# Kernel optimization log

Measured on AMD Instinct MI355X. Metric: run time of the kernel, lower is better.

The kernel has to match this reference:

```python
import jax, jax.numpy as jnp
import numpy as np

B, L, IN_DIM, H, KD = 2, 2048, 1024, 16, 64
SCALE = float(np.sqrt(IN_DIM / H))  # sqrt(in_dim / num_heads), per ScaledDotAttention
LN_EPS = 1e-5


def setup_inputs() -> dict:
    key = jax.random.key(0)
    ks = jax.random.split(key, 12)
    s_in = 1.0 / np.sqrt(IN_DIM)
    s_hd = 1.0 / np.sqrt(H * KD)
    return {
        "q": jax.random.normal(ks[0], (B, L, IN_DIM), jnp.float32),
        "k": jax.random.normal(ks[1], (B, L, IN_DIM), jnp.float32),
        "v": jax.random.normal(ks[2], (B, L, IN_DIM), jnp.float32),
        "Wq": jax.random.normal(ks[3], (IN_DIM, H * KD), jnp.float32) * s_in,
        "bq": jnp.zeros((H * KD,), jnp.float32),
        "Wk": jax.random.normal(ks[4], (IN_DIM, H * KD), jnp.float32) * s_in,
        "bk": jnp.zeros((H * KD,), jnp.float32),
        "Wv": jax.random.normal(ks[5], (IN_DIM, H * KD), jnp.float32) * s_in,
        "bv": jnp.zeros((H * KD,), jnp.float32),
        "Wo": jax.random.normal(ks[6], (H * KD, IN_DIM), jnp.float32) * s_hd,
        "bo": jnp.zeros((IN_DIM,), jnp.float32),
        "gamma": jnp.ones((IN_DIM,), jnp.float32),
        "beta": jnp.zeros((IN_DIM,), jnp.float32),
    }


def _split_heads(x):
    # [B, L, H*KD] -> [H*B, L, KD]  (heads MAJOR, matching permute(2,0,1,3).view)
    b, l, _ = x.shape
    return x.reshape(b, l, H, KD).transpose(2, 0, 1, 3).reshape(H * b, l, KD)


def reference(q, k, v, Wq, bq, Wk, bk, Wv, bv, Wo, bo, gamma, beta):
    res = q
    qh = _split_heads(q @ Wq + bq)   # [H*B, Lq, KD]
    kh = _split_heads(k @ Wk + bk)
    vh = _split_heads(v @ Wv + bv)
    scores = jnp.einsum("zqd,zkd->zqk", qh, kh) / SCALE
    atn = jax.nn.softmax(scores, axis=-1)          # [H*B, Lq, Lk]
    out = jnp.einsum("zqk,zkd->zqd", atn, vh)      # [H*B, Lq, KD]
    b = q.shape[0]
    out = out.reshape(H, b, -1, KD).transpose(1, 2, 0, 3).reshape(b, -1, H * KD)
    out = out @ Wo + bo
    x = out + res
    mu = jnp.mean(x, axis=-1, keepdims=True)
    var = jnp.mean(jnp.square(x - mu), axis=-1, keepdims=True)
    out = (x - mu) * jax.lax.rsqrt(var + LN_EPS) * gamma + beta
    return (out, atn)
```

## Files before the change

### kernel.cpp

```cpp
#include <hip/hip_runtime.h>
#include <hip/hip_bf16.h>

typedef unsigned short u16;
typedef unsigned int   u32;

using bf16x8 = __attribute__((ext_vector_type(8))) short;
using f32x4  = __attribute__((ext_vector_type(4))) float;

#define SEQ  2048
#define NZ   32
#define KTOT 1024
#define NTOT 1024
#define SC2  0.18033688011112042f

__device__ __forceinline__ u16 f2bf(float f) {
    union { float f; u32 u; } x; x.f = f;
    u32 r = x.u + 0x7fffu + ((x.u >> 16) & 1u);
    return (u16)(r >> 16);
}

__device__ __forceinline__ void gl_lds16(const u16* g, u16* ldsbase) {
    __builtin_amdgcn_global_load_lds(
        (const __attribute__((address_space(1))) u32*)g,
        (__attribute__((address_space(3))) u32*)ldsbase, 16, 0, 0);
}

__global__ __launch_bounds__(256) void prep_k(const float* __restrict__ q,
                                              const float* __restrict__ k,
                                              const float* __restrict__ v,
                                              const float* __restrict__ W0,
                                              const float* __restrict__ W1,
                                              const float* __restrict__ W2,
                                              const float* __restrict__ W3,
                                              u16* __restrict__ qb,
                                              u16* __restrict__ WT) {
    __shared__ u16 t[64 * 65];
    const int tid = threadIdx.x;
    const int b = blockIdx.x;
    if (b < 6144) {
        const int zc = b >> 11;
        const int xc = b & 2047;
        const float* src = (zc == 0) ? q : (zc == 1) ? k : v;
        u16* dst = qb + (size_t)zc * 4096 * 1024;
        int off = xc * 2048 + tid * 8;
        float4 v0 = *(const float4*)&src[off];
        float4 v1 = *(const float4*)&src[off + 4];
        uint4 o;
        o.x = (u32)f2bf(v0.x) | ((u32)f2bf(v0.y) << 16);
        o.y = (u32)f2bf(v0.z) | ((u32)f2bf(v0.w) << 16);
        o.z = (u32)f2bf(v1.x) | ((u32)f2bf(v1.y) << 16);
        o.w = (u32)f2bf(v1.z) | ((u32)f2bf(v1.w) << 16);
        *(uint4*)&dst[off] = o;
        return;
    }
    const int tt = b - 6144;
    const int zz = tt >> 8;
    const int bx = tt & 15, by = (tt >> 4) & 15;
    const float* W = (zz == 0) ? W0 : (zz == 1) ? W1 : (zz == 2) ? W2 : W3;
    u16* out = WT + (size_t)zz * 1024 * 1024;
    const int n0 = bx * 64, k0 = by * 64;
#pragma unroll
    for (int it = 0; it < 4; ++it) {
        int flat = it * 256 + tid;
        int r = flat >> 4, c4 = (flat & 15) * 4;
        float4 vv = *(const float4*)&W[(k0 + r) * 1024 + n0 + c4];
        t[r * 65 + c4 + 0] = f2bf(vv.x);
        t[r * 65 + c4 + 1] = f2bf(vv.y);
        t[r * 65 + c4 + 2] = f2bf(vv.z);
        t[r * 65 + c4 + 3] = f2bf(vv.w);
    }
    __syncthreads();
#pragma unroll
    for (int it = 0; it < 2; ++it) {
        int flat = it * 256 + tid;
        int rn = flat >> 3, c8 = (flat & 7) * 8;
        u32 p[4];
#pragma unroll
        for (int e = 0; e < 4; ++e) {
            u32 lo = t[(c8 + 2 * e + 0) * 65 + rn];
            u32 hi = t[(c8 + 2 * e + 1) * 65 + rn];
            p[e] = lo | (hi << 16);
        }
        uint4 o; o.x = p[0]; o.y = p[1]; o.z = p[2]; o.w = p[3];
        *(uint4*)&out[(n0 + rn) * 1024 + k0 + c8] = o;
    }
}

__global__ __launch_bounds__(256) void qkvproj_k(const u16* __restrict__ qb,
                                                 const u16* __restrict__ wt,
                                                 const float* __restrict__ bq,
                                                 const float* __restrict__ bk,
                                                 const float* __restrict__ bv,
                                                 u16* __restrict__ qh,
                                                 u16* __restrict__ kh,
                                                 u16* __restrict__ vhT) {
    __shared__ u16 As[128 * 32];
    __shared__ u16 Bs[128 * 32];
    __shared__ u16 T[128 * 132];
    const int zz = blockIdx.z;
    const u16*   A    = qb + (size_t)zz * 4096 * 1024;
    const u16*   WT   = wt + (size_t)zz * 1024 * 1024;
    const float* bias = (zz == 0) ? bq : (zz == 1) ? bk : bv;
    const bool vmode = (zz == 2);

    const int tid = threadIdx.x;
    const int m0 = blockIdx.y * 128;
    const int n0 = blockIdx.x * 128;
    const int wid = tid >> 6, lane = tid & 63;
    const int wrow = wid >> 1, wcol = wid & 1;
    const int g = lane >> 4, li = lane & 15;

    f32x4 acc[4][4];
#pragma unroll
    for (int a = 0; a < 4; ++a)
#pragma unroll
        for (int b = 0; b < 4; ++b) acc[a][b] = (f32x4){0.f, 0.f, 0.f, 0.f};

    for (int kt = 0; kt < KTOT / 32; ++kt) {
        const int kb = kt * 32;
#pragma unroll
        for (int cc = 0; cc < 2; ++cc) {
            int c = wid + cc * 4;
            gl_lds16(&A[(m0 + c * 16 + (lane >> 2)) * KTOT + kb + (lane & 3) * 8],
                     &As[c * 512]);
            gl_lds16(&WT[(n0 + c * 16 + (lane >> 2)) * KTOT + kb + (lane & 3) * 8],
                     &Bs[c * 512]);
        }
        __syncthreads();
        bf16x8 af[4], bfr[4];
#pragma unroll
        for (int fr = 0; fr < 4; ++fr)
            af[fr] = *(const bf16x8*)&As[(wrow * 64 + fr * 16 + li) * 32 + g * 8];
#pragma unroll
        for (int fc = 0; fc < 4; ++fc)
            bfr[fc] = *(const bf16x8*)&Bs[(wcol * 64 + fc * 16 + li) * 32 + g * 8];
#pragma unroll
        for (int fr = 0; fr < 4; ++fr)
#pragma unroll
            for (int fc = 0; fc < 4; ++fc)
                acc[fr][fc] = __builtin_amdgcn_mfma_f32_16x16x32_bf16(
                    af[fr], bfr[fc], acc[fr][fc], 0, 0, 0);
        __syncthreads();
    }

#pragma unroll
    for (int fr = 0; fr < 4; ++fr)
#pragma unroll
        for (int fc = 0; fc < 4; ++fc)
#pragma unroll
            for (int reg = 0; reg < 4; ++reg) {
                int rl = wrow * 64 + fr * 16 + g * 4 + reg;
                int cl = wcol * 64 + fc * 16 + li;
                u16 bv16 = f2bf(acc[fr][fc][reg] + bias[n0 + cl]);
                if (!vmode) T[rl * 132 + cl] = bv16;
                else        T[cl * 132 + rl] = bv16;
            }
    __syncthreads();

    const int bb2 = m0 >> 11, ml = m0 & 2047;
    const int lc8 = (tid & 7) * 8;
#pragma unroll
    for (int it = 0; it < 8; ++it) {
        int idx = it * 32 + (tid >> 3);
        int row = idx >> 1, half = idx & 1;
        uint4 val = *(const uint4*)&T[row * 132 + half * 64 + lc8];
        if (!vmode) {
            int h = (n0 >> 6) + half;
            u16* dst = (blockIdx.z == 0) ? qh : kh;
            *(uint4*)&dst[(((h * 2 + bb2) * 2048 + ml + row) << 6) + lc8] = val;
        } else {
            int cg = n0 + row;
            int h = cg >> 6, d = cg & 63;
            *(uint4*)&vhT[(((h * 2 + bb2) * 64 + d) << 11) + ml + half * 64 + lc8] = val;
        }
    }
}

__global__ __launch_bounds__(256) void outproj_k(const u16* __restrict__ A,
                                                 const u16* __restrict__ WT,
                                                 const float* __restrict__ bias,
                                                 const float* __restrict__ res,
                                                 float* __restrict__ outp) {
    __shared__ u16 As[128 * 32];
    __shared__ u16 Bs[128 * 32];
    const int tid = threadIdx.x;
    const int m0 = blockIdx.y * 128;
    const int n0 = blockIdx.x * 128;
    const int wid = tid >> 6, lane = tid & 63;
    const int wrow = wid >> 1, wcol = wid & 1;
    const int g = lane >> 4, li = lane & 15;

    f32x4 acc[4][4];
#pragma unroll
    for (int a = 0; a < 4; ++a)
#pragma unroll
        for (int b = 0; b < 4; ++b) acc[a][b] = (f32x4){0.f, 0.f, 0.f, 0.f};

    for (int kt = 0; kt < KTOT / 32; ++kt) {
        const int kb = kt * 32;
#pragma unroll
        for (int cc = 0; cc < 2; ++cc) {
            int c = wid + cc * 4;
            gl_lds16(&A[(m0 + c * 16 + (lane >> 2)) * KTOT + kb + (lane & 3) * 8],
                     &As[c * 512]);
            gl_lds16(&WT[(n0 + c * 16 + (lane >> 2)) * KTOT + kb + (lane & 3) * 8],
                     &Bs[c * 512]);
        }
        __syncthreads();
        bf16x8 af[4], bfr[4];
#pragma unroll
        for (int fr = 0; fr < 4; ++fr)
            af[fr] = *(const bf16x8*)&As[(wrow * 64 + fr * 16 + li) * 32 + g * 8];
#pragma unroll
        for (int fc = 0; fc < 4; ++fc)
            bfr[fc] = *(const bf16x8*)&Bs[(wcol * 64 + fc * 16 + li) * 32 + g * 8];
#pragma unroll
        for (int fr = 0; fr < 4; ++fr)
#pragma unroll
            for (int fc = 0; fc < 4; ++fc)
                acc[fr][fc] = __builtin_amdgcn_mfma_f32_16x16x32_bf16(
                    af[fr], bfr[fc], acc[fr][fc], 0, 0, 0);
        __syncthreads();
    }

#pragma unroll
    for (int fr = 0; fr < 4; ++fr)
#pragma unroll
        for (int fc = 0; fc < 4; ++fc)
#pragma unroll
            for (int reg = 0; reg < 4; ++reg) {
                int r = m0 + wrow * 64 + fr * 16 + g * 4 + reg;
                int c = n0 + wcol * 64 + fc * 16 + li;
                outp[r * NTOT + c] = acc[fr][fc][reg] + bias[c] + res[r * NTOT + c];
            }
}

__global__ __launch_bounds__(512) void attn_k(const u16* __restrict__ qh,
                                              const u16* __restrict__ kh,
                                              const u16* __restrict__ vhT,
                                              float* __restrict__ atn,
                                              u16* __restrict__ attnout) {
    __shared__ u16 lds[24576];
    const int tid = threadIdx.x;
    const int D = blockIdx.x;
    const int z = D & 31, q0 = (D >> 5) * 128;
    const int h = z >> 1, bb = z & 1;
    const int wid = tid >> 6, lane = tid & 63, g = lane >> 4, li = lane & 15;
    const int row0 = wid * 16;
    const int zbase = z * SEQ;
    const int swz = li & 7;

    bf16x8 aq[2];
#pragma unroll
    for (int ks = 0; ks < 2; ++ks)
        aq[ks] = *(const bf16x8*)
            &qh[(size_t)(zbase + q0 + row0 + li) * 64 + ks * 32 + g * 8];

    float lmv;
    {
        u16* KsA = lds;
        const int c0 = wid * 2, c1 = wid * 2 + 1;
        const int ar = lane >> 3;
        const int ac = (lane & 7) ^ ar;
        const u16* kA0 = &kh[(size_t)(zbase + c0 * 8 + ar) * 64 + ac * 8];
        const u16* kA1 = &kh[(size_t)(zbase + c1 * 8 + ar) * 64 + ac * 8];

        gl_lds16(kA0, &KsA[c0 * 512]);
        gl_lds16(kA1, &KsA[c1 * 512]);
        __syncthreads();

        float s = 0.f;
        for (int kt = 0; kt < 16; ++kt) {
            const int buf = kt & 1;
            if (kt < 15) {
                const size_t nxt = (size_t)(kt + 1) * 128 * 64;
                gl_lds16(kA0 + nxt, &KsA[(buf ^ 1) * 8192 + c0 * 512]);
                gl_lds16(kA1 + nxt, &KsA[(buf ^ 1) * 8192 + c1 * 512]);
            }
            f32x4 sv[8];
#pragma unroll
            for (int fc = 0; fc < 8; ++fc) sv[fc] = (f32x4){0.f, 0.f, 0.f, 0.f};
            __builtin_amdgcn_s_setprio(1);
#pragma unroll
            for (int ks = 0; ks < 2; ++ks) {
#pragma unroll
                for (int fc = 0; fc < 8; ++fc) {
                    bf16x8 kf = *(const bf16x8*)
                        &KsA[buf * 8192 + (fc * 16 + li) * 64 + (((ks * 4 + g) ^ swz) * 8)];
                    sv[fc] = __builtin_amdgcn_mfma_f32_16x16x32_bf16(
                        kf, aq[ks], sv[fc], 0, 0, 0);
                }
            }
            __builtin_amdgcn_s_setprio(0);
            float ssum = 0.f;
#pragma unroll
            for (int fc = 0; fc < 8; ++fc)
#pragma unroll
                for (int reg = 0; reg < 4; ++reg)
                    ssum += __builtin_amdgcn_exp2f(sv[fc][reg] * SC2);
            s += ssum;
            __syncthreads();
        }
        s += __shfl_xor(s, 16, 64);
        s += __shfl_xor(s, 32, 64);
        lmv = __builtin_amdgcn_logf(s);
    }

    u16* Ks = lds;
    u16* Vs = lds + 8192;
    u16* Ps = lds + 16384;
    const int srow = wid * 8 + (lane >> 3);
    const int schunk = (lane & 7) ^ (lane >> 3);
    const u16* ksrc = &kh[(size_t)(zbase + srow) * 64 + schunk * 8];
    const u16* vsrc = &vhT[(size_t)(z * 64 + srow) * SEQ + schunk * 8];

    gl_lds16(ksrc, &Ks[wid * 512]);
    gl_lds16(vsrc, &Vs[wid * 512]);
    __syncthreads();

    f32x4 oa[4];
#pragma unroll
    for (int fn = 0; fn < 4; ++fn) oa[fn] = (f32x4){0.f, 0.f, 0.f, 0.f};

    const u16* psw = &Ps[wid * 1024];
    const int prow = wid * 1024 + li * 64;
    for (int kt = 0; kt < 32; ++kt) {
        const int buf = kt & 1;
        const int k0 = kt * 64;
        if (kt < 31) {
            const size_t nxt = (size_t)((kt + 1) * 64);
            gl_lds16(ksrc + nxt * 64, &Ks[(buf ^ 1) * 4096 + wid * 512]);
            gl_lds16(vsrc + nxt, &Vs[(buf ^ 1) * 4096 + wid * 512]);
        }

        f32x4 sv[4];
#pragma unroll
        for (int fc = 0; fc < 4; ++fc) sv[fc] = (f32x4){0.f, 0.f, 0.f, 0.f};
        __builtin_amdgcn_s_setprio(1);
#pragma unroll
        for (int ks = 0; ks < 2; ++ks) {
#pragma unroll
            for (int fc = 0; fc < 4; ++fc) {
                bf16x8 kf = *(const bf16x8*)
                    &Ks[buf * 4096 + (fc * 16 + li) * 64 + (((ks * 4 + g) ^ swz) * 8)];
                sv[fc] = __builtin_amdgcn_mfma_f32_16x16x32_bf16(
                    kf, aq[ks], sv[fc], 0, 0, 0);
            }
        }
        __builtin_amdgcn_s_setprio(0);

#pragma unroll
        for (int fc = 0; fc < 4; ++fc) {
            float p0 = __builtin_amdgcn_exp2f(sv[fc][0] * SC2 - lmv);
            float p1 = __builtin_amdgcn_exp2f(sv[fc][1] * SC2 - lmv);
            float p2 = __builtin_amdgcn_exp2f(sv[fc][2] * SC2 - lmv);
            float p3 = __builtin_amdgcn_exp2f(sv[fc][3] * SC2 - lmv);
            u32 w0 = (u32)f2bf(p0) | ((u32)f2bf(p1) << 16);
            u32 w1 = (u32)f2bf(p2) | ((u32)f2bf(p3) << 16);
            int pc = ((fc * 2 + (g >> 1)) ^ swz) * 8 + (g & 1) * 4;
            *(u32*)&Ps[prow + pc]     = w0;
            *(u32*)&Ps[prow + pc + 2] = w1;
        }

#pragma unroll
        for (int it2 = 0; it2 < 4; ++it2) {
            int row  = it2 * 4 + (lane >> 4);
            int col8 = lane & 15;
            int lc   = col8 >> 1;
            uint2 d2 = *(const uint2*)
                &psw[row * 64 + ((lc ^ (row & 7)) << 3) + ((col8 & 1) << 2)];
            f32x4 o4;
            union { u32 u; float f; } c0v, c1v, c2v, c3v;
            c0v.u = (d2.x & 0xffffu) << 16;  c1v.u = d2.x & 0xffff0000u;
            c2v.u = (d2.y & 0xffffu) << 16;  c3v.u = d2.y & 0xffff0000u;
            o4[0] = c0v.f; o4[1] = c1v.f; o4[2] = c2v.f; o4[3] = c3v.f;
            __builtin_nontemporal_store(o4, (f32x4*)
                &atn[(size_t)(zbase + q0 + row0 + row) * SEQ + k0 + col8 * 4]);
        }

        __builtin_amdgcn_s_setprio(1);
#pragma unroll
        for (int ks = 0; ks < 2; ++ks) {
            bf16x8 pf = *(const bf16x8*)&Ps[prow + (((ks * 4 + g) ^ swz) * 8)];
#pragma unroll
            for (int fn = 0; fn < 4; ++fn) {
                bf16x8 vf = *(const bf16x8*)
                    &Vs[buf * 4096 + (fn * 16 + li) * 64 + (((ks * 4 + g) ^ swz) * 8)];
                oa[fn] = __builtin_amdgcn_mfma_f32_16x16x32_bf16(
                    vf, pf, oa[fn], 0, 0, 0);
            }
        }
        __builtin_amdgcn_s_setprio(0);
        asm volatile("s_waitcnt vmcnt(4) lgkmcnt(0)" ::: "memory");
        __builtin_amdgcn_s_barrier();
    }

#pragma unroll
    for (int fn = 0; fn < 4; ++fn) {
        u32 w0 = (u32)f2bf(oa[fn][0]) | ((u32)f2bf(oa[fn][1]) << 16);
        u32 w1 = (u32)f2bf(oa[fn][2]) | ((u32)f2bf(oa[fn][3]) << 16);
        uint2 wv; wv.x = w0; wv.y = w1;
        *(uint2*)&attnout[(size_t)(bb * SEQ + q0 + row0 + li) * 1024
                          + h * 64 + fn * 16 + g * 4] = wv;
    }
}

__global__ __launch_bounds__(256) void ln_k(const float* __restrict__ y,
                                            const float* __restrict__ gamma,
                                            const float* __restrict__ beta,
                                            float* __restrict__ out) {
    __shared__ float red[8];
    const int row = blockIdx.x, tid = threadIdx.x;
    float4 v = *(const float4*)&y[row * 1024 + tid * 4];
    float s = v.x + v.y + v.z + v.w;
    float sq = v.x * v.x + v.y * v.y + v.z * v.z + v.w * v.w;
#pragma unroll
    for (int msk = 1; msk <= 32; msk <<= 1) {
        s += __shfl_xor(s, msk, 64);
        sq += __shfl_xor(sq, msk, 64);
    }
    const int wid = tid >> 6;
    if ((tid & 63) == 0) { red[wid * 2] = s; red[wid * 2 + 1] = sq; }
    __syncthreads();
    s = red[0] + red[2] + red[4] + red[6];
    sq = red[1] + red[3] + red[5] + red[7];
    float mu = s * (1.0f / 1024.0f);
    float var = sq * (1.0f / 1024.0f) - mu * mu;
    float rs = rsqrtf(var + 1e-5f);
    float4 g4 = *(const float4*)&gamma[tid * 4];
    float4 b4 = *(const float4*)&beta[tid * 4];
    float4 o;
    o.x = (v.x - mu) * rs * g4.x + b4.x;
    o.y = (v.y - mu) * rs * g4.y + b4.y;
    o.z = (v.z - mu) * rs * g4.z + b4.z;
    o.w = (v.w - mu) * rs * g4.w + b4.w;
    *(float4*)&out[row * 1024 + tid * 4] = o;
}

extern "C" void kernel_launch(void* const* d_in, const int* in_sizes, int n_in,
                              void* d_out, int out_size, void* d_ws, size_t ws_size,
                              hipStream_t stream) {
    const float* q     = (const float*)d_in[0];
    const float* k     = (const float*)d_in[1];
    const float* v     = (const float*)d_in[2];
    const float* Wq    = (const float*)d_in[3];
    const float* bq    = (const float*)d_in[4];
    const float* Wk    = (const float*)d_in[5];
    const float* bk    = (const float*)d_in[6];
    const float* Wv    = (const float*)d_in[7];
    const float* bv    = (const float*)d_in[8];
    const float* Wo    = (const float*)d_in[9];
    const float* bo    = (const float*)d_in[10];
    const float* gamma = (const float*)d_in[11];
    const float* beta  = (const float*)d_in[12];

    float* out = (float*)d_out;
    float* atn = out + 4096 * 1024;

    u16* wt  = (u16*)d_ws;
    u16* qb  = wt + 4 * 1024 * 1024;
    u16* attnout = qb;
    float* y = (float*)(qb + 4096 * 1024);
    u16* qh  = qb + 3 * 4096 * 1024;
    u16* kh  = qh + NZ * SEQ * 64;
    u16* vhT = kh + NZ * SEQ * 64;
    u16* wto = wt + 3 * 1024 * 1024;

    dim3 tb(256);
    prep_k<<<dim3(7168), tb, 0, stream>>>(q, k, v, Wq, Wk, Wv, Wo, qb, wt);

    qkvproj_k<<<dim3(8, 32, 3), tb, 0, stream>>>(qb, wt, bq, bk, bv,
                                                 qh, kh, vhT);

    attn_k<<<dim3(512), dim3(512), 0, stream>>>(qh, kh, vhT, atn, attnout);

    outproj_k<<<dim3(8, 32), tb, 0, stream>>>(attnout, wto, bo, q, y);

    ln_k<<<dim3(4096), tb, 0, stream>>>(y, gamma, beta, out);
}
```

Measured before the change: 262.1 us.

## Load K/V fragments directly into registers and process two query sets per warp

The attention kernel stops staging K and V tiles in LDS through global_load_lds with barriers. Each warp now loads K/V MFMA fragments straight from global memory into registers, prefetching the next tile. Each warp handles 32 query rows (two 16-row sets) so every loaded K/V fragment feeds two MFMA streams, and the grid halves to 256 blocks with occupancy 2. This removes block-wide barriers and LDS traffic, but it increases global/L2 loads per warp and register pressure, and exposes fewer blocks on a large GPU.

```diff
diff --git a/kernel.cpp b/kernel.cpp
--- a/kernel.cpp
+++ b/kernel.cpp
@@ -23,6 +23,47 @@
     __builtin_amdgcn_global_load_lds(
         (const __attribute__((address_space(1))) u32*)g,
         (__attribute__((address_space(3))) u32*)ldsbase, 16, 0, 0);
+}
+
+__device__ __forceinline__ void ldk8(bf16x8 (&dst)[2][4], const u16* kbase,
+                                     int krow0, int klo) {
+#pragma unroll
+    for (int ks = 0; ks < 2; ++ks)
+#pragma unroll
+        for (int fc = 0; fc < 4; ++fc)
+            dst[ks][fc] = *(const bf16x8*)
+                &kbase[(size_t)(krow0 + fc * 16) * 64 + ks * 32 + klo];
+}
+
+__device__ __forceinline__ void passa_half(const bf16x8 (&kr)[2][4],
+                                           const bf16x8 (&aq)[2][2],
+                                           float& s0, float& s1) {
+    f32x4 sv0[4], sv1[4];
+#pragma unroll
+    for (int fc = 0; fc < 4; ++fc) {
+        sv0[fc] = (f32x4){0.f, 0.f, 0.f, 0.f};
+        sv1[fc] = (f32x4){0.f, 0.f, 0.f, 0.f};
+    }
+    __builtin_amdgcn_s_setprio(1);
+#pragma unroll
+    for (int ks = 0; ks < 2; ++ks)
+#pragma unroll
+        for (int fc = 0; fc < 4; ++fc) {
+            sv0[fc] = __builtin_amdgcn_mfma_f32_16x16x32_bf16(
+                kr[ks][fc], aq[0][ks], sv0[fc], 0, 0, 0);
+            sv1[fc] = __builtin_amdgcn_mfma_f32_16x16x32_bf16(
+                kr[ks][fc], aq[1][ks], sv1[fc], 0, 0, 0);
+        }
+    __builtin_amdgcn_s_setprio(0);
+    float a0 = 0.f, a1 = 0.f;
+#pragma unroll
+    for (int fc = 0; fc < 4; ++fc)
+#pragma unroll
+        for (int reg = 0; reg < 4; ++reg) {
+            a0 += __builtin_amdgcn_exp2f(sv0[fc][reg] * SC2);
+            a1 += __builtin_amdgcn_exp2f(sv1[fc][reg] * SC2);
+        }
+    s0 += a0; s1 += a1;
 }
 
 __global__ __launch_bounds__(256) void prep_k(const float* __restrict__ q,
@@ -235,174 +276,178 @@
             }
 }
 
-__global__ __launch_bounds__(512) void attn_k(const u16* __restrict__ qh,
-                                              const u16* __restrict__ kh,
-                                              const u16* __restrict__ vhT,
-                                              float* __restrict__ atn,
-                                              u16* __restrict__ attnout) {
-    __shared__ u16 lds[24576];
+__global__ __launch_bounds__(512, 2) void attn_k(const u16* __restrict__ qh,
+                                                 const u16* __restrict__ kh,
+                                                 const u16* __restrict__ vhT,
+                                                 float* __restrict__ atn,
+                                                 u16* __restrict__ attnout) {
+    __shared__ u16 Ps[8 * 2048];
     const int tid = threadIdx.x;
     const int D = blockIdx.x;
-    const int z = D & 31, q0 = (D >> 5) * 128;
+    const int z = D & 31, q0 = (D >> 5) * 256;
     const int h = z >> 1, bb = z & 1;
     const int wid = tid >> 6, lane = tid & 63, g = lane >> 4, li = lane & 15;
-    const int row0 = wid * 16;
+    const int row0 = wid * 32;
     const int zbase = z * SEQ;
     const int swz = li & 7;
 
-    bf16x8 aq[2];
-#pragma unroll
-    for (int ks = 0; ks < 2; ++ks)
-        aq[ks] = *(const bf16x8*)
-            &qh[(size_t)(zbase + q0 + row0 + li) * 64 + ks * 32 + g * 8];
-
-    float lmv;
+    const u16* kbase = kh + (size_t)zbase * 64;
+    const u16* vbase = vhT + (size_t)(z * 64) * SEQ;
+    const int klo = li * 64 + g * 8;
+    const int vlo = li * SEQ + g * 8;
+
+    bf16x8 aq[2][2];
+#pragma unroll
+    for (int set = 0; set < 2; ++set)
+#pragma unroll
+        for (int ks = 0; ks < 2; ++ks)
+            aq[set][ks] = *(const bf16x8*)
+                &qh[(size_t)(zbase + q0 + row0 + set * 16 + li) * 64
+                    + ks * 32 + g * 8];
+
+    float lmv0, lmv1;
     {
-        u16* KsA = lds;
-        const int c0 = wid * 2, c1 = wid * 2 + 1;
-        const int ar = lane >> 3;
-        const int ac = (lane & 7) ^ ar;
-        const u16* kA0 = &kh[(size_t)(zbase + c0 * 8 + ar) * 64 + ac * 8];
-        const u16* kA1 = &kh[(size_t)(zbase + c1 * 8 + ar) * 64 + ac * 8];
-
-        gl_lds16(kA0, &KsA[c0 * 512]);
-        gl_lds16(kA1, &KsA[c1 * 512]);
-        __syncthreads();
-
-        float s = 0.f;
-        for (int kt = 0; kt < 16; ++kt) {
-            const int buf = kt & 1;
-            if (kt < 15) {
-                const size_t nxt = (size_t)(kt + 1) * 128 * 64;
-                gl_lds16(kA0 + nxt, &KsA[(buf ^ 1) * 8192 + c0 * 512]);
-                gl_lds16(kA1 + nxt, &KsA[(buf ^ 1) * 8192 + c1 * 512]);
-            }
-            f32x4 sv[8];
-#pragma unroll
-            for (int fc = 0; fc < 8; ++fc) sv[fc] = (f32x4){0.f, 0.f, 0.f, 0.f};
-            __builtin_amdgcn_s_setprio(1);
-#pragma unroll
-            for (int ks = 0; ks < 2; ++ks) {
-#pragma unroll
-                for (int fc = 0; fc < 8; ++fc) {
-                    bf16x8 kf = *(const bf16x8*)
-                        &KsA[buf * 8192 + (fc * 16 + li) * 64 + (((ks * 4 + g) ^ swz) * 8)];
-                    sv[fc] = __builtin_amdgcn_mfma_f32_16x16x32_bf16(
-                        kf, aq[ks], sv[fc], 0, 0, 0);
-                }
-            }
-            __builtin_amdgcn_s_setprio(0);
-            float ssum = 0.f;
-#pragma unroll
-            for (int fc = 0; fc < 8; ++fc)
-#pragma unroll
-                for (int reg = 0; reg < 4; ++reg)
-                    ssum += __builtin_amdgcn_exp2f(sv[fc][reg] * SC2);
-            s += ssum;
-            __syncthreads();
-        }
-        s += __shfl_xor(s, 16, 64);
-        s += __shfl_xor(s, 32, 64);
-        lmv = __builtin_amdgcn_logf(s);
-    }
-
-    u16* Ks = lds;
-    u16* Vs = lds + 8192;
-    u16* Ps = lds + 16384;
-    const int srow = wid * 8 + (lane >> 3);
-    const int schunk = (lane & 7) ^ (lane >> 3);
-    const u16* ksrc = &kh[(size_t)(zbase + srow) * 64 + schunk * 8];
-    const u16* vsrc = &vhT[(size_t)(z * 64 + srow) * SEQ + schunk * 8];
-
-    gl_lds16(ksrc, &Ks[wid * 512]);
-    gl_lds16(vsrc, &Vs[wid * 512]);
-    __syncthreads();
-
-    f32x4 oa[4];
-#pragma unroll
-    for (int fn = 0; fn < 4; ++fn) oa[fn] = (f32x4){0.f, 0.f, 0.f, 0.f};
-
-    const u16* psw = &Ps[wid * 1024];
-    const int prow = wid * 1024 + li * 64;
+        float s0 = 0.f, s1 = 0.f;
+        bf16x8 ka[2][4], kb[2][4];
+        ldk8(ka, kbase, 0, klo);
+        for (int kt = 0; kt < 32; kt += 2) {
+            ldk8(kb, kbase, (kt + 1) * 64, klo);
+            passa_half(ka, aq, s0, s1);
+            if (kt < 30) ldk8(ka, kbase, (kt + 2) * 64, klo);
+            passa_half(kb, aq, s0, s1);
+        }
+        s0 += __shfl_xor(s0, 16, 64);
+        s0 += __shfl_xor(s0, 32, 64);
+        s1 += __shfl_xor(s1, 16, 64);
+        s1 += __shfl_xor(s1, 32, 64);
+        lmv0 = __builtin_amdgcn_logf(s0);
+        lmv1 = __builtin_amdgcn_logf(s1);
+    }
+
+    f32x4 oa[2][4];
+#pragma unroll
+    for (int set = 0; set < 2; ++set)
+#pragma unroll
+        for (int fn = 0; fn < 4; ++fn) oa[set][fn] = (f32x4){0.f, 0.f, 0.f, 0.f};
+
+    const int prow0 = wid * 2048 + li * 64;
+    const int prow1 = prow0 + 1024;
+    const int pswb  = wid * 2048;
+
+    bf16x8 kf[2][4], vf[2][4];
+    ldk8(kf, kbase, 0, klo);
+
     for (int kt = 0; kt < 32; ++kt) {
-        const int buf = kt & 1;
         const int k0 = kt * 64;
-        if (kt < 31) {
-            const size_t nxt = (size_t)((kt + 1) * 64);
-            gl_lds16(ksrc + nxt * 64, &Ks[(buf ^ 1) * 4096 + wid * 512]);
-            gl_lds16(vsrc + nxt, &Vs[(buf ^ 1) * 4096 + wid * 512]);
-        }
 
         f32x4 sv[4];
 #pragma unroll
         for (int fc = 0; fc < 4; ++fc) sv[fc] = (f32x4){0.f, 0.f, 0.f, 0.f};
         __builtin_amdgcn_s_setprio(1);
 #pragma unroll
-        for (int ks = 0; ks < 2; ++ks) {
-#pragma unroll
-            for (int fc = 0; fc < 4; ++fc) {
-                bf16x8 kf = *(const bf16x8*)
-                    &Ks[buf * 4096 + (fc * 16 + li) * 64 + (((ks * 4 + g) ^ swz) * 8)];
+        for (int ks = 0; ks < 2; ++ks)
+#pragma unroll
+            for (int fc = 0; fc < 4; ++fc)
                 sv[fc] = __builtin_amdgcn_mfma_f32_16x16x32_bf16(
-                    kf, aq[ks], sv[fc], 0, 0, 0);
-            }
-        }
+                    kf[ks][fc], aq[0][ks], sv[fc], 0, 0, 0);
         __builtin_amdgcn_s_setprio(0);
-
 #pragma unroll
         for (int fc = 0; fc < 4; ++fc) {
-            float p0 = __builtin_amdgcn_exp2f(sv[fc][0] * SC2 - lmv);
-            float p1 = __builtin_amdgcn_exp2f(sv[fc][1] * SC2 - lmv);
-            float p2 = __builtin_amdgcn_exp2f(sv[fc][2] * SC2 - lmv);
-            float p3 = __builtin_amdgcn_exp2f(sv[fc][3] * SC2 - lmv);
+            float p0 = __builtin_amdgcn_exp2f(sv[fc][0] * SC2 - lmv0);
+            float p1 = __builtin_amdgcn_exp2f(sv[fc][1] * SC2 - lmv0);
+            float p2 = __builtin_amdgcn_exp2f(sv[fc][2] * SC2 - lmv0);
+            float p3 = __builtin_amdgcn_exp2f(sv[fc][3] * SC2 - lmv0);
             u32 w0 = (u32)f2bf(p0) | ((u32)f2bf(p1) << 16);
             u32 w1 = (u32)f2bf(p2) | ((u32)f2bf(p3) << 16);
             int pc = ((fc * 2 + (g >> 1)) ^ swz) * 8 + (g & 1) * 4;
-            *(u32*)&Ps[prow + pc]     = w0;
-            *(u32*)&Ps[prow + pc + 2] = w1;
-        }
-
-#pragma unroll
-        for (int it2 = 0; it2 < 4; ++it2) {
-            int row  = it2 * 4 + (lane >> 4);
-            int col8 = lane & 15;
-            int lc   = col8 >> 1;
-            uint2 d2 = *(const uint2*)
-                &psw[row * 64 + ((lc ^ (row & 7)) << 3) + ((col8 & 1) << 2)];
-            f32x4 o4;
-            union { u32 u; float f; } c0v, c1v, c2v, c3v;
-            c0v.u = (d2.x & 0xffffu) << 16;  c1v.u = d2.x & 0xffff0000u;
-            c2v.u = (d2.y & 0xffffu) << 16;  c3v.u = d2.y & 0xffff0000u;
-            o4[0] = c0v.f; o4[1] = c1v.f; o4[2] = c2v.f; o4[3] = c3v.f;
-            __builtin_nontemporal_store(o4, (f32x4*)
-                &atn[(size_t)(zbase + q0 + row0 + row) * SEQ + k0 + col8 * 4]);
-        }
-
+            *(u32*)&Ps[prow0 + pc]     = w0;
+            *(u32*)&Ps[prow0 + pc + 2] = w1;
+        }
+
+        f32x4 sw[4];
+#pragma unroll
+        for (int fc = 0; fc < 4; ++fc) sw[fc] = (f32x4){0.f, 0.f, 0.f, 0.f};
         __builtin_amdgcn_s_setprio(1);
 #pragma unroll
+        for (int ks = 0; ks < 2; ++ks)
+#pragma unroll
+            for (int fc = 0; fc < 4; ++fc)
+                sw[fc] = __builtin_amdgcn_mfma_f32_16x16x32_bf16(
+                    kf[ks][fc], aq[1][ks], sw[fc], 0, 0, 0);
+        __builtin_amdgcn_s_setprio(0);
+
+#pragma unroll
+        for (int ks = 0; ks < 2; ++ks)
+#pragma unroll
+            for (int fn = 0; fn < 4; ++fn)
+                vf[ks][fn] = *(const bf16x8*)
+                    &vbase[(size_t)(fn * 16) * SEQ + vlo + k0 + ks * 32];
+        if (kt < 31) ldk8(kf, kbase, k0 + 64, klo);
+
+#pragma unroll
+        for (int fc = 0; fc < 4; ++fc) {
+            float p0 = __builtin_amdgcn_exp2f(sw[fc][0] * SC2 - lmv1);
+            float p1 = __builtin_amdgcn_exp2f(sw[fc][1] * SC2 - lmv1);
+            float p2 = __builtin_amdgcn_exp2f(sw[fc][2] * SC2 - lmv1);
+            float p3 = __builtin_amdgcn_exp2f(sw[fc][3] * SC2 - lmv1);
+            u32 w0 = (u32)f2bf(p0) | ((u32)f2bf(p1) << 16);
+            u32 w1 = (u32)f2bf(p2) | ((u32)f2bf(p3) << 16);
+            int pc = ((fc * 2 + (g >> 1)) ^ swz) * 8 + (g & 1) * 4;
+            *(u32*)&Ps[prow1 + pc]     = w0;
+            *(u32*)&Ps[prow1 + pc + 2] = w1;
+        }
+
+#pragma unroll
+        for (int set = 0; set < 2; ++set) {
+#pragma unroll
+            for (int it2 = 0; it2 < 4; ++it2) {
+                int row  = it2 * 4 + (lane >> 4);
+                int col8 = lane & 15;
+                int lc   = col8 >> 1;
+                uint2 d2 = *(const uint2*)
+                    &Ps[pswb + set * 1024 + row * 64
+                        + ((lc ^ (row & 7)) << 3) + ((col8 & 1) << 2)];
+                f32x4 o4;
+                union { u32 u; float f; } c0v, c1v, c2v, c3v;
+                c0v.u = (d2.x & 0xffffu) << 16;  c1v.u = d2.x & 0xffff0000u;
+                c2v.u = (d2.y & 0xffffu) << 16;  c3v.u = d2.y & 0xffff0000u;
+                o4[0] = c0v.f; o4[1] = c1v.f; o4[2] = c2v.f; o4[3] = c3v.f;
+                __builtin_nontemporal_store(o4, (f32x4*)
+                    &atn[(size_t)(zbase + q0 + row0 + set * 16 + row) * SEQ
+                         + k0 + col8 * 4]);
+            }
+        }
+
+        __builtin_amdgcn_s_setprio(1);
+#pragma unroll
         for (int ks = 0; ks < 2; ++ks) {
-            bf16x8 pf = *(const bf16x8*)&Ps[prow + (((ks * 4 + g) ^ swz) * 8)];
-#pragma unroll
-            for (int fn = 0; fn < 4; ++fn) {
-                bf16x8 vf = *(const bf16x8*)
-                    &Vs[buf * 4096 + (fn * 16 + li) * 64 + (((ks * 4 + g) ^ swz) * 8)];
-                oa[fn] = __builtin_amdgcn_mfma_f32_16x16x32_bf16(
-                    vf, pf, oa[fn], 0, 0, 0);
-            }
+            bf16x8 pf0 = *(const bf16x8*)&Ps[prow0 + (((ks * 4 + g) ^ swz) * 8)];
+#pragma unroll
+            for (int fn = 0; fn < 4; ++fn)
+                oa[0][fn] = __builtin_amdgcn_mfma_f32_16x16x32_bf16(
+                    vf[ks][fn], pf0, oa[0][fn], 0, 0, 0);
+        }
+#pragma unroll
+        for (int ks = 0; ks < 2; ++ks) {
+            bf16x8 pf1 = *(const bf16x8*)&Ps[prow1 + (((ks * 4 + g) ^ swz) * 8)];
+#pragma unroll
+            for (int fn = 0; fn < 4; ++fn)
+                oa[1][fn] = __builtin_amdgcn_mfma_f32_16x16x32_bf16(
+                    vf[ks][fn], pf1, oa[1][fn], 0, 0, 0);
         }
         __builtin_amdgcn_s_setprio(0);
-        asm volatile("s_waitcnt vmcnt(4) lgkmcnt(0)" ::: "memory");
-        __builtin_amdgcn_s_barrier();
-    }
-
-#pragma unroll
-    for (int fn = 0; fn < 4; ++fn) {
-        u32 w0 = (u32)f2bf(oa[fn][0]) | ((u32)f2bf(oa[fn][1]) << 16);
-        u32 w1 = (u32)f2bf(oa[fn][2]) | ((u32)f2bf(oa[fn][3]) << 16);
-        uint2 wv; wv.x = w0; wv.y = w1;
-        *(uint2*)&attnout[(size_t)(bb * SEQ + q0 + row0 + li) * 1024
-                          + h * 64 + fn * 16 + g * 4] = wv;
-    }
+    }
+
+#pragma unroll
+    for (int set = 0; set < 2; ++set)
+#pragma unroll
+        for (int fn = 0; fn < 4; ++fn) {
+            u32 w0 = (u32)f2bf(oa[set][fn][0]) | ((u32)f2bf(oa[set][fn][1]) << 16);
+            u32 w1 = (u32)f2bf(oa[set][fn][2]) | ((u32)f2bf(oa[set][fn][3]) << 16);
+            uint2 wv; wv.x = w0; wv.y = w1;
+            *(uint2*)&attnout[(size_t)(bb * SEQ + q0 + row0 + set * 16 + li) * 1024
+                              + h * 64 + fn * 16 + g * 4] = wv;
+        }
 }
 
 __global__ __launch_bounds__(256) void ln_k(const float* __restrict__ y,
@@ -472,7 +517,7 @@
     qkvproj_k<<<dim3(8, 32, 3), tb, 0, stream>>>(qb, wt, bq, bk, bv,
                                                  qh, kh, vhT);
 
-    attn_k<<<dim3(512), dim3(512), 0, stream>>>(qh, kh, vhT, atn, attnout);
+    attn_k<<<dim3(256), dim3(512), 0, stream>>>(qh, kh, vhT, atn, attnout);
 
     outproj_k<<<dim3(8, 32), tb, 0, stream>>>(attnout, wto, bo, q, y);
 
```

Result: slower. 293.6 us (+12.0%).

## Load V fragments directly from global into registers, shrink LDS footprint

Applied to the files above, without the earlier changes.

Removes the LDS staging buffer for V: each lane now loads its V MFMA fragments straight from global memory into registers inside the loop, issued early so they overlap with the softmax and probability writes. LDS drops from 48KB to 32KB and launch bounds now request 4 blocks per CU, aiming for higher occupancy and fewer LDS reads. The vmcnt wait is raised to account for the extra outstanding loads. The cost is uncoalesced, strided global reads for V on every tile and more register pressure, with global latency exposed close to the MFMAs.

```diff
diff --git a/kernel.cpp b/kernel.cpp
--- a/kernel.cpp
+++ b/kernel.cpp
@@ -235,12 +235,12 @@
             }
 }
 
-__global__ __launch_bounds__(512) void attn_k(const u16* __restrict__ qh,
-                                              const u16* __restrict__ kh,
-                                              const u16* __restrict__ vhT,
-                                              float* __restrict__ atn,
-                                              u16* __restrict__ attnout) {
-    __shared__ u16 lds[24576];
+__global__ __launch_bounds__(512, 4) void attn_k(const u16* __restrict__ qh,
+                                                 const u16* __restrict__ kh,
+                                                 const u16* __restrict__ vhT,
+                                                 float* __restrict__ atn,
+                                                 u16* __restrict__ attnout) {
+    __shared__ u16 lds[16384];
     const int tid = threadIdx.x;
     const int D = blockIdx.x;
     const int z = D & 31, q0 = (D >> 5) * 128;
@@ -307,15 +307,14 @@
     }
 
     u16* Ks = lds;
-    u16* Vs = lds + 8192;
-    u16* Ps = lds + 16384;
+    u16* Ps = lds + 8192;
     const int srow = wid * 8 + (lane >> 3);
     const int schunk = (lane & 7) ^ (lane >> 3);
     const u16* ksrc = &kh[(size_t)(zbase + srow) * 64 + schunk * 8];
-    const u16* vsrc = &vhT[(size_t)(z * 64 + srow) * SEQ + schunk * 8];
+    const u16* vbase = vhT + (size_t)(z * 64) * SEQ;
+    const int vlo = li * SEQ + g * 8;
 
     gl_lds16(ksrc, &Ks[wid * 512]);
-    gl_lds16(vsrc, &Vs[wid * 512]);
     __syncthreads();
 
     f32x4 oa[4];
@@ -330,7 +329,6 @@
         if (kt < 31) {
             const size_t nxt = (size_t)((kt + 1) * 64);
             gl_lds16(ksrc + nxt * 64, &Ks[(buf ^ 1) * 4096 + wid * 512]);
-            gl_lds16(vsrc + nxt, &Vs[(buf ^ 1) * 4096 + wid * 512]);
         }
 
         f32x4 sv[4];
@@ -348,6 +346,12 @@
             }
         }
         __builtin_amdgcn_s_setprio(0);
+
+        bf16x8 vf0[4];
+#pragma unroll
+        for (int fn = 0; fn < 4; ++fn)
+            vf0[fn] = *(const bf16x8*)
+                &vbase[(size_t)(fn * 16) * SEQ + vlo + k0];
 
 #pragma unroll
         for (int fc = 0; fc < 4; ++fc) {
@@ -361,6 +365,12 @@
             *(u32*)&Ps[prow + pc]     = w0;
             *(u32*)&Ps[prow + pc + 2] = w1;
         }
+
+        bf16x8 vf1[4];
+#pragma unroll
+        for (int fn = 0; fn < 4; ++fn)
+            vf1[fn] = *(const bf16x8*)
+                &vbase[(size_t)(fn * 16) * SEQ + vlo + k0 + 32];
 
 #pragma unroll
         for (int it2 = 0; it2 < 4; ++it2) {
@@ -379,19 +389,20 @@
         }
 
         __builtin_amdgcn_s_setprio(1);
-#pragma unroll
-        for (int ks = 0; ks < 2; ++ks) {
-            bf16x8 pf = *(const bf16x8*)&Ps[prow + (((ks * 4 + g) ^ swz) * 8)];
-#pragma unroll
-            for (int fn = 0; fn < 4; ++fn) {
-                bf16x8 vf = *(const bf16x8*)
-                    &Vs[buf * 4096 + (fn * 16 + li) * 64 + (((ks * 4 + g) ^ swz) * 8)];
+        {
+            bf16x8 pf0 = *(const bf16x8*)&Ps[prow + ((g ^ swz) * 8)];
+#pragma unroll
+            for (int fn = 0; fn < 4; ++fn)
                 oa[fn] = __builtin_amdgcn_mfma_f32_16x16x32_bf16(
-                    vf, pf, oa[fn], 0, 0, 0);
-            }
+                    vf0[fn], pf0, oa[fn], 0, 0, 0);
+            bf16x8 pf1 = *(const bf16x8*)&Ps[prow + (((4 + g) ^ swz) * 8)];
+#pragma unroll
+            for (int fn = 0; fn < 4; ++fn)
+                oa[fn] = __builtin_amdgcn_mfma_f32_16x16x32_bf16(
+                    vf1[fn], pf1, oa[fn], 0, 0, 0);
         }
         __builtin_amdgcn_s_setprio(0);
-        asm volatile("s_waitcnt vmcnt(4) lgkmcnt(0)" ::: "memory");
+        asm volatile("s_waitcnt vmcnt(8) lgkmcnt(0)" ::: "memory");
         __builtin_amdgcn_s_barrier();
     }
 
```

Measured after the change: 312.8 us. 19.3% more time.
